# Kernel tuning notes

Hardware: AMD Instinct MI355X
Metric: run time of the kernel (lower is better)

The kernel has to match this reference:

```python
import jax, jax.numpy as jnp
import numpy as np

B, T, V = 32, 100, 20000
E, H, M, DD = 128, 128, 64, 2


def setup_inputs() -> dict:
    key = jax.random.key(0)
    ks = jax.random.split(key, 12)
    x = jax.random.uniform(ks[0], (B, T, V), dtype=jnp.float32)
    # zero out trailing timesteps per example so Masking layer matters
    lens = jax.random.randint(ks[1], (B,), T * 3 // 4, T + 1)
    tmask = (jnp.arange(T)[None, :] < lens[:, None]).astype(jnp.float32)
    x = x * tmask[:, :, None]
    a = jax.random.uniform(ks[2], (B, V), dtype=jnp.float32)
    d = jax.random.normal(ks[3], (B, DD), dtype=jnp.float32)
    # parameters
    emb = jax.random.uniform(ks[4], (V, E), minval=-0.1, maxval=0.1, dtype=jnp.float32)
    s = 1.0 / np.sqrt(E)
    gru_k = jax.random.uniform(ks[5], (E, 3 * H), minval=-s, maxval=s, dtype=jnp.float32)
    gru_rk = jax.random.normal(ks[6], (H, 3 * H), dtype=jnp.float32) / np.sqrt(H)
    gru_b_i = jnp.zeros((3 * H,), jnp.float32)   # input bias (reset_after=True)
    gru_b_r = jnp.zeros((3 * H,), jnp.float32)   # recurrent bias
    s1 = 1.0 / np.sqrt(H + E)
    W1 = jax.random.uniform(ks[7], (H + E, M), minval=-s1, maxval=s1, dtype=jnp.float32)
    b1 = jnp.zeros((M,), jnp.float32)
    s2 = 1.0 / np.sqrt(M + DD)
    W2 = jax.random.uniform(ks[8], (M + DD, 1), minval=-s2, maxval=s2, dtype=jnp.float32)
    b2 = jnp.zeros((1,), jnp.float32)
    return dict(x=x, a=a, d=d, emb=emb, gru_k=gru_k, gru_rk=gru_rk,
                gru_b_i=gru_b_i, gru_b_r=gru_b_r, W1=W1, b1=b1, W2=W2, b2=b2)


def _gru_final_state(xe, mask, gru_k, gru_rk, gru_b_i, gru_b_r):
    # xe: [B,T,E], mask: [B,T] bool. Keras GRU, reset_after=True, eval mode (dropout off).
    Hn = gru_rk.shape[0]
    x_proj = jnp.einsum('bte,eh->bth', xe, gru_k) + gru_b_i  # [B,T,3H]

    def step(h, inp):
        xp_t, m_t = inp                      # [B,3H], [B]
        rec = h @ gru_rk + gru_b_r           # [B,3H]
        xz, xr, xh = jnp.split(xp_t, 3, axis=-1)
        rz, rr, rh = jnp.split(rec, 3, axis=-1)
        z = jax.nn.sigmoid(xz + rz)
        r = jax.nn.sigmoid(xr + rr)
        hh = jnp.tanh(xh + r * rh)
        h_new = z * h + (1.0 - z) * hh
        h = jnp.where(m_t[:, None], h_new, h)  # masked steps carry state
        return h, None

    h0 = jnp.zeros((xe.shape[0], Hn), xe.dtype)
    h_final, _ = jax.lax.scan(step, h0, (jnp.swapaxes(x_proj, 0, 1), jnp.swapaxes(mask, 0, 1)))
    return h_final


def reference(x, a, d, emb, gru_k, gru_rk, gru_b_i, gru_b_r, W1, b1, W2, b2):
    ae = jnp.tanh(a @ emb)                       # [B,E]
    xe = jnp.tanh(jnp.einsum('btv,ve->bte', x, emb))  # [B,T,E]
    mask = jnp.any(xe != 0.0, axis=-1)           # Masking(mask_value=0.0)
    h = _gru_final_state(xe, mask, gru_k, gru_rk, gru_b_i, gru_b_r)  # [B,H]
    c = jnp.tanh(jnp.concatenate([h, ae], axis=1) @ W1 + b1)         # [B,M]
    out = jax.nn.sigmoid(jnp.concatenate([c, d], axis=1) @ W2 + b2)  # [B,1]
    return out
```

## Files before the change

kernel.cpp:

```cpp
#include <hip/hip_runtime.h>

typedef __attribute__((ext_vector_type(8))) short short8;
typedef __attribute__((ext_vector_type(4))) float float4v;

#define V_ 20000

__device__ __forceinline__ unsigned short f2bf(float f) {
    union { float f; unsigned int u; } v; v.f = f;
    unsigned int u = v.u;
    u += 0x7fffu + ((u >> 16) & 1u);
    return (unsigned short)(u >> 16);
}

__device__ __forceinline__ float fast_tanh(float x) {
    float xc = fminf(15.f, fmaxf(-15.f, x));
    float e = __expf(2.f * xc);
    return (e - 1.f) / (e + 1.f);
}

__device__ __forceinline__ float sigmoidf_(float x) {
    float xc = fminf(30.f, fmaxf(-30.f, x));
    return 1.f / (1.f + __expf(-xc));
}

#define GLL16(gp, lp) __builtin_amdgcn_global_load_lds( \
    (const __attribute__((address_space(1))) void*)(gp), \
    (__attribute__((address_space(3))) void*)(lp), 16, 0, 0)

__global__ __launch_bounds__(256) void cvt_embT(const float* __restrict__ emb,
                                                unsigned short* __restrict__ embT) {
    __shared__ unsigned short tile[128 * 65];
    int tid = threadIdx.x;
    int k0 = blockIdx.x * 64;
    const float4v* e4 = (const float4v*)emb;
    #pragma unroll
    for (int c = 0; c < 8; ++c) {
        int l4 = c * 256 + tid;
        int k = l4 >> 5;
        int n4 = l4 & 31;
        float4v f = {0.f, 0.f, 0.f, 0.f};
        if (k0 + k < V_) f = e4[(size_t)(k0 + k) * 32 + n4];
        tile[(n4 * 4 + 0) * 65 + k] = f2bf(f.x);
        tile[(n4 * 4 + 1) * 65 + k] = f2bf(f.y);
        tile[(n4 * 4 + 2) * 65 + k] = f2bf(f.z);
        tile[(n4 * 4 + 3) * 65 + k] = f2bf(f.w);
    }
    __syncthreads();
    #pragma unroll
    for (int c = 0; c < 4; ++c) {
        int l8 = c * 256 + tid;
        int n = l8 >> 3, seg = l8 & 7;
        int kk = k0 + seg * 8;
        if (kk < V_) {
            short8 v;
            #pragma unroll
            for (int i = 0; i < 8; ++i) v[i] = (short)tile[n * 65 + seg * 8 + i];
            *(short8*)(embT + (size_t)n * V_ + kk) = v;
        }
    }
}

__global__ __launch_bounds__(256, 4) void big_gemm(const float* __restrict__ x,
                                                   const float* __restrict__ a,
                                                   const unsigned short* __restrict__ embT,
                                                   float* __restrict__ partial,
                                                   int ks) {
    __shared__ unsigned short Alds[2][128 * 40];
    __shared__ unsigned short Blds[2][128 * 32];
    int tid = threadIdx.x;
    int bx = blockIdx.x, by = blockIdx.y;
    int m0 = bx * 128;
    int per = 625 / ks, extra = 625 % ks;
    int kb0 = by * per + (by < extra ? by : extra);
    int nkb = per + (by < extra ? 1 : 0);

    int lane = tid & 63, wave = tid >> 6;
    int wr = wave >> 1, wc = wave & 1;
    int ln = lane & 15, quad = lane >> 4;

    float4v acc[4][4];
    #pragma unroll
    for (int i = 0; i < 4; ++i)
        #pragma unroll
        for (int j = 0; j < 4; ++j) acc[i][j] = (float4v){0.f, 0.f, 0.f, 0.f};

    int row = tid >> 1, seg = tid & 1;
    int rg = m0 + row;
    int aidx = rg - 3200; aidx = aidx < 0 ? 0 : (aidx > 31 ? 31 : aidx);
    const float* __restrict__ srcA = (rg < 3200) ? (x + (size_t)rg * V_)
                                                 : (a + (size_t)aidx * V_);
    int brow0 = tid >> 2, bkq = tid & 3;
    int wbase = tid & ~63;
    const unsigned short* gB0 = embT + (size_t)brow0 * V_ + bkq * 8;
    const unsigned short* gB1 = embT + (size_t)(64 + brow0) * V_ + bkq * 8;

    float4v fa0, fa1, fa2, fa3;

    {
        int k0 = kb0 * 32;
        const float4v* ap = (const float4v*)(srcA + k0 + seg * 16);
        fa0 = ap[0]; fa1 = ap[1]; fa2 = ap[2]; fa3 = ap[3];
        GLL16(gB0 + k0, &Blds[0][(size_t)wbase * 8]);
        GLL16(gB1 + k0, &Blds[0][(size_t)(256 + wbase) * 8]);
        short8 w0, w1;
        w0[0]=(short)f2bf(fa0.x); w0[1]=(short)f2bf(fa0.y); w0[2]=(short)f2bf(fa0.z); w0[3]=(short)f2bf(fa0.w);
        w0[4]=(short)f2bf(fa1.x); w0[5]=(short)f2bf(fa1.y); w0[6]=(short)f2bf(fa1.z); w0[7]=(short)f2bf(fa1.w);
        w1[0]=(short)f2bf(fa2.x); w1[1]=(short)f2bf(fa2.y); w1[2]=(short)f2bf(fa2.z); w1[3]=(short)f2bf(fa2.w);
        w1[4]=(short)f2bf(fa3.x); w1[5]=(short)f2bf(fa3.y); w1[6]=(short)f2bf(fa3.z); w1[7]=(short)f2bf(fa3.w);
        *(short8*)&Alds[0][row * 40 + seg * 16]     = w0;
        *(short8*)&Alds[0][row * 40 + seg * 16 + 8] = w1;
    }
    __syncthreads();

    for (int it = 0; it < nkb; ++it) {
        int buf = it & 1, nxt = buf ^ 1;
        bool more = (it + 1 < nkb);
        if (more) {
            int k0 = (kb0 + it + 1) * 32;
            const float4v* ap = (const float4v*)(srcA + k0 + seg * 16);
            fa0 = ap[0]; fa1 = ap[1]; fa2 = ap[2]; fa3 = ap[3];
            GLL16(gB0 + k0, &Blds[nxt][(size_t)wbase * 8]);
            GLL16(gB1 + k0, &Blds[nxt][(size_t)(256 + wbase) * 8]);
        }
        short8 af[4];
        #pragma unroll
        for (int i = 0; i < 4; ++i)
            af[i] = *(const short8*)&Alds[buf][(wr * 64 + i * 16 + ln) * 40 + quad * 8];
        #pragma unroll
        for (int j = 0; j < 4; ++j) {
            short8 bf = *(const short8*)&Blds[buf][(wc * 64 + j * 16 + ln) * 32 + quad * 8];
            #pragma unroll
            for (int i = 0; i < 4; ++i)
                acc[i][j] = __builtin_amdgcn_mfma_f32_16x16x32_bf16(af[i], bf, acc[i][j], 0, 0, 0);
        }
        if (more) {
            short8 w0, w1;
            w0[0]=(short)f2bf(fa0.x); w0[1]=(short)f2bf(fa0.y); w0[2]=(short)f2bf(fa0.z); w0[3]=(short)f2bf(fa0.w);
            w0[4]=(short)f2bf(fa1.x); w0[5]=(short)f2bf(fa1.y); w0[6]=(short)f2bf(fa1.z); w0[7]=(short)f2bf(fa1.w);
            w1[0]=(short)f2bf(fa2.x); w1[1]=(short)f2bf(fa2.y); w1[2]=(short)f2bf(fa2.z); w1[3]=(short)f2bf(fa2.w);
            w1[4]=(short)f2bf(fa3.x); w1[5]=(short)f2bf(fa3.y); w1[6]=(short)f2bf(fa3.z); w1[7]=(short)f2bf(fa3.w);
            *(short8*)&Alds[nxt][row * 40 + seg * 16]     = w0;
            *(short8*)&Alds[nxt][row * 40 + seg * 16 + 8] = w1;
        }
        __syncthreads();
    }

    float* dst = partial + (size_t)by * 3328 * 128;
    #pragma unroll
    for (int i = 0; i < 4; ++i) {
        #pragma unroll
        for (int j = 0; j < 4; ++j) {
            int rowb = m0 + wr * 64 + i * 16 + quad * 4;
            int col = wc * 64 + j * 16 + ln;
            #pragma unroll
            for (int r = 0; r < 4; ++r)
                dst[(size_t)(rowb + r) * 128 + col] = acc[i][j][r];
        }
    }
}

__global__ __launch_bounds__(128) void reduce_tanh(const float* __restrict__ partial,
                                                   float* __restrict__ xe,
                                                   float* __restrict__ ae,
                                                   float* __restrict__ maskg,
                                                   int ks) {
    int row = blockIdx.x;
    int e = threadIdx.x;
    float s = 0.f;
    for (int k = 0; k < ks; ++k)
        s += partial[((size_t)k * 3328 + row) * 128 + e];
    float v = fast_tanh(s);
    if (row < 3200) {
        xe[(size_t)row * 128 + e] = v;
        __shared__ int any;
        if (e == 0) any = 0;
        __syncthreads();
        if (v != 0.f) any = 1;
        __syncthreads();
        if (e == 0) maskg[row] = any ? 1.f : 0.f;
    } else {
        ae[(row - 3200) * 128 + e] = v;
    }
}

__global__ __launch_bounds__(384) void xproj_kernel(const float* __restrict__ xe,
                                                    const float* __restrict__ gru_k,
                                                    const float* __restrict__ b_i,
                                                    float* __restrict__ xproj) {
    __shared__ float xs[16 * 128];
    int tid = threadIdx.x;
    int row0 = blockIdx.x * 16;
    const float4v* src = (const float4v*)(xe + (size_t)row0 * 128);
    float4v* dstl = (float4v*)xs;
    #pragma unroll
    for (int c = 0; c < 2; ++c) {
        int i4 = c * 384 + tid;
        if (i4 < 512) dstl[i4] = src[i4];
    }
    __syncthreads();
    int j = tid;
    float acc[16];
    #pragma unroll
    for (int r = 0; r < 16; ++r) acc[r] = 0.f;
    float bi = b_i[j];
    for (int k4 = 0; k4 < 32; ++k4) {
        float g0 = gru_k[(k4 * 4 + 0) * 384 + j];
        float g1 = gru_k[(k4 * 4 + 1) * 384 + j];
        float g2 = gru_k[(k4 * 4 + 2) * 384 + j];
        float g3 = gru_k[(k4 * 4 + 3) * 384 + j];
        #pragma unroll
        for (int r = 0; r < 16; ++r) {
            float4v xv = *(const float4v*)&xs[r * 128 + k4 * 4];
            acc[r] = fmaf(xv.x, g0, acc[r]);
            acc[r] = fmaf(xv.y, g1, acc[r]);
            acc[r] = fmaf(xv.z, g2, acc[r]);
            acc[r] = fmaf(xv.w, g3, acc[r]);
        }
    }
    #pragma unroll
    for (int r = 0; r < 16; ++r)
        xproj[(size_t)(row0 + r) * 384 + j] = acc[r] + bi;
}

__global__ __launch_bounds__(384) void gru_kernel(const float* __restrict__ xproj,
                                                  const float* __restrict__ maskg,
                                                  const float* __restrict__ gru_rk,
                                                  const float* __restrict__ b_r,
                                                  float* __restrict__ hout) {
    int b = blockIdx.x;
    int j = threadIdx.x;
    float w[128];
    #pragma unroll
    for (int k = 0; k < 128; ++k) w[k] = gru_rk[k * 384 + j];
    float br = b_r[j];
    __shared__ float4v hs4[32];
    __shared__ float recs[384];
    float* hs = (float*)hs4;
    float hreg = 0.f;
    if (j < 128) hs[j] = 0.f;
    const float* xp_base = xproj + (size_t)b * 100 * 384;
    const float* mk = maskg + b * 100;
    float xz = 0.f, xr = 0.f, xh = 0.f;
    if (j < 128) { xz = xp_base[j]; xr = xp_base[128 + j]; xh = xp_base[256 + j]; }
    __syncthreads();
    for (int t = 0; t < 100; ++t) {
        float nxz = 0.f, nxr = 0.f, nxh = 0.f;
        if (t < 99 && j < 128) {
            const float* nb = xp_base + (t + 1) * 384;
            nxz = nb[j]; nxr = nb[128 + j]; nxh = nb[256 + j];
        }
        float s0 = 0.f, s1 = 0.f, s2 = 0.f, s3 = 0.f;
        #pragma unroll
        for (int k4 = 0; k4 < 32; ++k4) {
            float4v hv = hs4[k4];
            s0 = fmaf(hv.x, w[k4 * 4 + 0], s0);
            s1 = fmaf(hv.y, w[k4 * 4 + 1], s1);
            s2 = fmaf(hv.z, w[k4 * 4 + 2], s2);
            s3 = fmaf(hv.w, w[k4 * 4 + 3], s3);
        }
        recs[j] = br + ((s0 + s1) + (s2 + s3));
        __syncthreads();
        if (j < 128) {
            float z = sigmoidf_(xz + recs[j]);
            float r = sigmoidf_(xr + recs[128 + j]);
            float hh = fast_tanh(xh + r * recs[256 + j]);
            float hn = z * hreg + (1.f - z) * hh;
            hreg = (mk[t] != 0.f) ? hn : hreg;
            hs[j] = hreg;
        }
        __syncthreads();
        xz = nxz; xr = nxr; xh = nxh;
    }
    if (j < 128) hout[b * 128 + j] = hreg;
}

__global__ __launch_bounds__(64) void head_kernel(const float* __restrict__ hout,
                                                  const float* __restrict__ ae,
                                                  const float* __restrict__ d,
                                                  const float* __restrict__ W1,
                                                  const float* __restrict__ b1,
                                                  const float* __restrict__ W2,
                                                  const float* __restrict__ b2,
                                                  float* __restrict__ out) {
    int b = blockIdx.x;
    int m = threadIdx.x;
    float s = b1[m];
    const float* hb = hout + b * 128;
    const float* ab = ae + b * 128;
    #pragma unroll 4
    for (int k = 0; k < 128; ++k) s = fmaf(hb[k], W1[k * 64 + m], s);
    #pragma unroll 4
    for (int k = 0; k < 128; ++k) s = fmaf(ab[k], W1[(128 + k) * 64 + m], s);
    float c = fast_tanh(s);
    float p = c * W2[m];
    #pragma unroll
    for (int off = 32; off > 0; off >>= 1) p += __shfl_down(p, off);
    if (m == 0) {
        p += d[b * 2 + 0] * W2[64] + d[b * 2 + 1] * W2[65] + b2[0];
        out[b] = sigmoidf_(p);
    }
}

extern "C" void kernel_launch(void* const* d_in, const int* in_sizes, int n_in,
                              void* d_out, int out_size, void* d_ws, size_t ws_size,
                              hipStream_t stream) {
    (void)in_sizes; (void)n_in; (void)out_size;
    const float* x      = (const float*)d_in[0];
    const float* a      = (const float*)d_in[1];
    const float* d      = (const float*)d_in[2];
    const float* emb    = (const float*)d_in[3];
    const float* gru_k  = (const float*)d_in[4];
    const float* gru_rk = (const float*)d_in[5];
    const float* gbi    = (const float*)d_in[6];
    const float* gbr    = (const float*)d_in[7];
    const float* W1     = (const float*)d_in[8];
    const float* b1     = (const float*)d_in[9];
    const float* W2     = (const float*)d_in[10];
    const float* b2     = (const float*)d_in[11];
    float* out = (float*)d_out;

    char* ws = (char*)d_ws;
    unsigned short* embT = (unsigned short*)(ws);
    float* xe      = (float*)(ws + 5120000);
    float* ae      = (float*)(ws + 6758400);
    float* maskg   = (float*)(ws + 6774784);
    float* xproj   = (float*)(ws + 6787584);
    float* hout    = (float*)(ws + 11702784);
    const size_t fixed = 11719168;
    const size_t slice = (size_t)3328 * 128 * 4;
    float* partial = (float*)(ws + fixed);

    int ks = 8;
    if (ws_size > fixed + slice) {
        size_t avail = (ws_size - fixed) / slice;
        ks = (int)(avail < 32 ? avail : 32);
        if (ks < 1) ks = 1;
    }

    hipLaunchKernelGGL(cvt_embT,    dim3(313),     dim3(256), 0, stream, emb, embT);
    hipLaunchKernelGGL(big_gemm,    dim3(26, ks),  dim3(256), 0, stream, x, a, embT, partial, ks);
    hipLaunchKernelGGL(reduce_tanh, dim3(3232),    dim3(128), 0, stream, partial, xe, ae, maskg, ks);
    hipLaunchKernelGGL(xproj_kernel,dim3(200),     dim3(384), 0, stream, xe, gru_k, gbi, xproj);
    hipLaunchKernelGGL(gru_kernel,  dim3(32),      dim3(384), 0, stream, xproj, maskg, gru_rk, gbr, hout);
    hipLaunchKernelGGL(head_kernel, dim3(32),      dim3(64),  0, stream, hout, ae, d, W1, b1, W2, b2, out);
}
```

Baseline: 572.2 us.

## Replace split-K partial buffers with atomic accumulation and fuse reduce and head kernels

The split-K GEMM now accumulates directly into one zeroed buffer with atomic adds, and the embedding conversion kernel performs that zeroing. This removes the per-slice partial buffers and the separate reduce pass. The tanh and mask computation moves into the xproj kernel, with an extra block handling ae, and the head MLP is folded into the end of the GRU kernel, cutting two launches and an intermediate round trip. In exchange the summation order becomes nondeterministic, atomics contend on the output, and ks is fixed at 32.

```diff
diff --git a/kernel.cpp b/kernel.cpp
--- a/kernel.cpp
+++ b/kernel.cpp
@@ -28,9 +28,13 @@
     (__attribute__((address_space(3))) void*)(lp), 16, 0, 0)
 
 __global__ __launch_bounds__(256) void cvt_embT(const float* __restrict__ emb,
-                                                unsigned short* __restrict__ embT) {
+                                                unsigned short* __restrict__ embT,
+                                                float* __restrict__ xeacc) {
+    int tid = threadIdx.x;
+    int gid = blockIdx.x * 256 + tid;
+    for (int i = gid; i < 3328 * 128; i += 313 * 256) xeacc[i] = 0.f;
+
     __shared__ unsigned short tile[128 * 65];
-    int tid = threadIdx.x;
     int k0 = blockIdx.x * 64;
     const float4v* e4 = (const float4v*)emb;
     #pragma unroll
@@ -63,7 +67,7 @@
 __global__ __launch_bounds__(256, 4) void big_gemm(const float* __restrict__ x,
                                                    const float* __restrict__ a,
                                                    const unsigned short* __restrict__ embT,
-                                                   float* __restrict__ partial,
+                                                   float* __restrict__ xeacc,
                                                    int ks) {
     __shared__ unsigned short Alds[2][128 * 40];
     __shared__ unsigned short Blds[2][128 * 32];
@@ -145,7 +149,6 @@
         __syncthreads();
     }
 
-    float* dst = partial + (size_t)by * 3328 * 128;
     #pragma unroll
     for (int i = 0; i < 4; ++i) {
         #pragma unroll
@@ -154,50 +157,36 @@
             int col = wc * 64 + j * 16 + ln;
             #pragma unroll
             for (int r = 0; r < 4; ++r)
-                dst[(size_t)(rowb + r) * 128 + col] = acc[i][j][r];
-        }
-    }
-}
-
-__global__ __launch_bounds__(128) void reduce_tanh(const float* __restrict__ partial,
-                                                   float* __restrict__ xe,
-                                                   float* __restrict__ ae,
+                unsafeAtomicAdd(&xeacc[(size_t)(rowb + r) * 128 + col], acc[i][j][r]);
+        }
+    }
+}
+
+__global__ __launch_bounds__(384) void xproj_fused(const float* __restrict__ xeacc,
+                                                   const float* __restrict__ gru_k,
+                                                   const float* __restrict__ b_i,
+                                                   float* __restrict__ xproj,
                                                    float* __restrict__ maskg,
-                                                   int ks) {
-    int row = blockIdx.x;
-    int e = threadIdx.x;
-    float s = 0.f;
-    for (int k = 0; k < ks; ++k)
-        s += partial[((size_t)k * 3328 + row) * 128 + e];
-    float v = fast_tanh(s);
-    if (row < 3200) {
-        xe[(size_t)row * 128 + e] = v;
-        __shared__ int any;
-        if (e == 0) any = 0;
-        __syncthreads();
-        if (v != 0.f) any = 1;
-        __syncthreads();
-        if (e == 0) maskg[row] = any ? 1.f : 0.f;
-    } else {
-        ae[(row - 3200) * 128 + e] = v;
-    }
-}
-
-__global__ __launch_bounds__(384) void xproj_kernel(const float* __restrict__ xe,
-                                                    const float* __restrict__ gru_k,
-                                                    const float* __restrict__ b_i,
-                                                    float* __restrict__ xproj) {
+                                                   float* __restrict__ ae) {
+    int tid = threadIdx.x;
+    if (blockIdx.x == 200) {
+        for (int i = tid; i < 32 * 128; i += 384)
+            ae[i] = fast_tanh(xeacc[3200 * 128 + i]);
+        return;
+    }
     __shared__ float xs[16 * 128];
-    int tid = threadIdx.x;
+    __shared__ int anyr[16];
     int row0 = blockIdx.x * 16;
-    const float4v* src = (const float4v*)(xe + (size_t)row0 * 128);
-    float4v* dstl = (float4v*)xs;
-    #pragma unroll
-    for (int c = 0; c < 2; ++c) {
-        int i4 = c * 384 + tid;
-        if (i4 < 512) dstl[i4] = src[i4];
-    }
-    __syncthreads();
+    if (tid < 16) anyr[tid] = 0;
+    __syncthreads();
+    for (int i = tid; i < 2048; i += 384) {
+        float v = fast_tanh(xeacc[(size_t)row0 * 128 + i]);
+        xs[i] = v;
+        if (v != 0.f) anyr[i >> 7] = 1;
+    }
+    __syncthreads();
+    if (tid < 16) maskg[row0 + tid] = anyr[tid] ? 1.f : 0.f;
+
     int j = tid;
     float acc[16];
     #pragma unroll
@@ -222,11 +211,17 @@
         xproj[(size_t)(row0 + r) * 384 + j] = acc[r] + bi;
 }
 
-__global__ __launch_bounds__(384) void gru_kernel(const float* __restrict__ xproj,
-                                                  const float* __restrict__ maskg,
-                                                  const float* __restrict__ gru_rk,
-                                                  const float* __restrict__ b_r,
-                                                  float* __restrict__ hout) {
+__global__ __launch_bounds__(384) void gru_fused(const float* __restrict__ xproj,
+                                                 const float* __restrict__ maskg,
+                                                 const float* __restrict__ gru_rk,
+                                                 const float* __restrict__ b_r,
+                                                 const float* __restrict__ ae,
+                                                 const float* __restrict__ d,
+                                                 const float* __restrict__ W1,
+                                                 const float* __restrict__ b1,
+                                                 const float* __restrict__ W2,
+                                                 const float* __restrict__ b2,
+                                                 float* __restrict__ out) {
     int b = blockIdx.x;
     int j = threadIdx.x;
     float w[128];
@@ -271,40 +266,29 @@
         __syncthreads();
         xz = nxz; xr = nxr; xh = nxh;
     }
-    if (j < 128) hout[b * 128 + j] = hreg;
-}
-
-__global__ __launch_bounds__(64) void head_kernel(const float* __restrict__ hout,
-                                                  const float* __restrict__ ae,
-                                                  const float* __restrict__ d,
-                                                  const float* __restrict__ W1,
-                                                  const float* __restrict__ b1,
-                                                  const float* __restrict__ W2,
-                                                  const float* __restrict__ b2,
-                                                  float* __restrict__ out) {
-    int b = blockIdx.x;
-    int m = threadIdx.x;
-    float s = b1[m];
-    const float* hb = hout + b * 128;
-    const float* ab = ae + b * 128;
-    #pragma unroll 4
-    for (int k = 0; k < 128; ++k) s = fmaf(hb[k], W1[k * 64 + m], s);
-    #pragma unroll 4
-    for (int k = 0; k < 128; ++k) s = fmaf(ab[k], W1[(128 + k) * 64 + m], s);
-    float c = fast_tanh(s);
-    float p = c * W2[m];
-    #pragma unroll
-    for (int off = 32; off > 0; off >>= 1) p += __shfl_down(p, off);
-    if (m == 0) {
-        p += d[b * 2 + 0] * W2[64] + d[b * 2 + 1] * W2[65] + b2[0];
-        out[b] = sigmoidf_(p);
+    if (j < 64) {
+        int m = j;
+        float s = b1[m];
+        const float* ab = ae + b * 128;
+        #pragma unroll 4
+        for (int k = 0; k < 128; ++k) s = fmaf(hs[k], W1[k * 64 + m], s);
+        #pragma unroll 4
+        for (int k = 0; k < 128; ++k) s = fmaf(ab[k], W1[(128 + k) * 64 + m], s);
+        float c = fast_tanh(s);
+        float p = c * W2[m];
+        #pragma unroll
+        for (int off = 32; off > 0; off >>= 1) p += __shfl_down(p, off);
+        if (m == 0) {
+            p += d[b * 2 + 0] * W2[64] + d[b * 2 + 1] * W2[65] + b2[0];
+            out[b] = sigmoidf_(p);
+        }
     }
 }
 
 extern "C" void kernel_launch(void* const* d_in, const int* in_sizes, int n_in,
                               void* d_out, int out_size, void* d_ws, size_t ws_size,
                               hipStream_t stream) {
-    (void)in_sizes; (void)n_in; (void)out_size;
+    (void)in_sizes; (void)n_in; (void)out_size; (void)ws_size;
     const float* x      = (const float*)d_in[0];
     const float* a      = (const float*)d_in[1];
     const float* d      = (const float*)d_in[2];
@@ -321,26 +305,16 @@
 
     char* ws = (char*)d_ws;
     unsigned short* embT = (unsigned short*)(ws);
-    float* xe      = (float*)(ws + 5120000);
-    float* ae      = (float*)(ws + 6758400);
-    float* maskg   = (float*)(ws + 6774784);
-    float* xproj   = (float*)(ws + 6787584);
-    float* hout    = (float*)(ws + 11702784);
-    const size_t fixed = 11719168;
-    const size_t slice = (size_t)3328 * 128 * 4;
-    float* partial = (float*)(ws + fixed);
-
-    int ks = 8;
-    if (ws_size > fixed + slice) {
-        size_t avail = (ws_size - fixed) / slice;
-        ks = (int)(avail < 32 ? avail : 32);
-        if (ks < 1) ks = 1;
-    }
-
-    hipLaunchKernelGGL(cvt_embT,    dim3(313),     dim3(256), 0, stream, emb, embT);
-    hipLaunchKernelGGL(big_gemm,    dim3(26, ks),  dim3(256), 0, stream, x, a, embT, partial, ks);
-    hipLaunchKernelGGL(reduce_tanh, dim3(3232),    dim3(128), 0, stream, partial, xe, ae, maskg, ks);
-    hipLaunchKernelGGL(xproj_kernel,dim3(200),     dim3(384), 0, stream, xe, gru_k, gbi, xproj);
-    hipLaunchKernelGGL(gru_kernel,  dim3(32),      dim3(384), 0, stream, xproj, maskg, gru_rk, gbr, hout);
-    hipLaunchKernelGGL(head_kernel, dim3(32),      dim3(64),  0, stream, hout, ae, d, W1, b1, W2, b2, out);
-}
+    float* xeacc   = (float*)(ws + 5120000);
+    float* ae      = (float*)(ws + 6823936);
+    float* maskg   = (float*)(ws + 6840320);
+    float* xproj   = (float*)(ws + 6853120);
+
+    const int ks = 32;
+
+    hipLaunchKernelGGL(cvt_embT,    dim3(313),    dim3(256), 0, stream, emb, embT, xeacc);
+    hipLaunchKernelGGL(big_gemm,    dim3(26, ks), dim3(256), 0, stream, x, a, embT, xeacc, ks);
+    hipLaunchKernelGGL(xproj_fused, dim3(201),    dim3(384), 0, stream, xeacc, gru_k, gbi, xproj, maskg, ae);
+    hipLaunchKernelGGL(gru_fused,   dim3(32),     dim3(384), 0, stream, xproj, maskg, gru_rk, gbr,
+                       ae, d, W1, b1, W2, b2, out);
+}
```

Result: no change. 573.4 us (+0.2%).
